# Kernel optimization log

Measured on AMD Instinct MI355X. Metric: run time of the kernel, lower is better.

## Reference

```python
import jax, jax.numpy as jnp
import numpy as np

B, N, P, K, D = 8, 2048, 64, 32, 384
DEPTH, DI, DS, DCONV, DTR, NC = 12, 768, 16, 4, 24, 40
BN_EPS = 1e-5


def _spread_bits(v):
    v = v & 1023
    v = (v | (v << 16)) & 50331903
    v = (v | (v << 8)) & 50393103
    v = (v | (v << 4)) & 51130563
    v = (v | (v << 2)) & 153391689
    return v


def _zkey(x, y, z):
    return _spread_bits(x) | (_spread_bits(y) << 1) | (_spread_bits(z) << 2)


def _sfc_order(xyz, trans):
    lo = xyz.min(0, keepdims=True)
    hi = xyz.max(0, keepdims=True)
    q = jnp.clip(((xyz - lo) / (hi - lo + 1e-6) * 1023.0).astype(jnp.int32), 0, 1023)
    if trans:
        keys = _zkey(q[:, 2], q[:, 1], q[:, 0])
    else:
        keys = _zkey(q[:, 0], q[:, 1], q[:, 2])
    return jnp.argsort(keys)


def _ln(x, g, b):
    m = x.mean(-1, keepdims=True)
    v = jnp.var(x, axis=-1, keepdims=True)
    return (x - m) / jnp.sqrt(v + 1e-5) * g + b


def _bn_eval(x, g, b):
    # BatchNorm in eval mode, running_mean=0 / running_var=1
    return x * (g / np.float32(np.sqrt(1.0 + BN_EPS))) + b


def _patch_embed_one(xyz, w1, b1, g1, be1, w2, b2, g2, be2, w3, b3, g3, be3):
    # xyz: (N,3)
    cidx = (jnp.arange(P) * (N / P)).astype(jnp.int32)
    centers = xyz[cidx]                                      # (P,3)
    d2 = ((centers[:, None, :] - xyz[None, :, :]) ** 2).sum(-1)  # (P,N)
    _, knn = jax.lax.top_k(-d2, K)                           # (P,K) smallest dists
    nx = xyz[knn] - centers[:, None, :]                      # (P,K,3)
    h = jax.nn.gelu(_bn_eval(nx @ w1.T + b1, g1, be1), approximate=False)   # (P,K,64)
    h = jax.nn.gelu(_bn_eval(h @ w2.T + b2, g2, be2), approximate=False)    # (P,K,128)
    h = _bn_eval(h @ w3.T + b3, g3, be3)                     # (P,K,384)
    return h.max(1), centers


def _mamba(x, in_w, conv_w, conv_b, xp_w, dt_w, dt_b, Alog, Dp, out_w):
    # x: (B,L,D)
    Bsz, L, _ = x.shape
    xz = x @ in_w.T                                          # (B,L,2*DI)
    xc, z = xz[..., :DI], xz[..., DI:]
    xpad = jnp.pad(xc, ((0, 0), (DCONV - 1, 0), (0, 0)))
    xc = sum(xpad[:, j:j + L, :] * conv_w[:, j] for j in range(DCONV)) + conv_b
    xc = jax.nn.silu(xc)
    x_dbl = xc @ xp_w.T                                      # (B,L,DTR+2*DS)
    dt = x_dbl[..., :DTR]
    Bm = x_dbl[..., DTR:DTR + DS]
    Cm = x_dbl[..., DTR + DS:]
    delta = jax.nn.softplus(dt @ dt_w.T + dt_b)              # (B,L,DI)
    A = -jnp.exp(Alog)                                       # (DI,DS)

    def step(h, inp):
        d_t, B_t, C_t, u_t = inp                             # (B,DI),(B,DS),(B,DS),(B,DI)
        h = h * jnp.exp(d_t[..., None] * A) + (d_t * u_t)[..., None] * B_t[:, None, :]
        return h, jnp.einsum('bds,bs->bd', h, C_t)

    h0 = jnp.zeros((Bsz, DI, DS), x.dtype)
    inps = (delta.transpose(1, 0, 2), Bm.transpose(1, 0, 2),
            Cm.transpose(1, 0, 2), xc.transpose(1, 0, 2))
    _, ys = jax.lax.scan(step, h0, inps)                     # (L,B,DI)
    y = ys.transpose(1, 0, 2) + Dp * xc
    y = y * jax.nn.silu(z)
    return y @ out_w.T


def setup_inputs() -> dict:
    key = jax.random.key(0)
    ks = iter(jax.random.split(key, 64))
    nrm = lambda *s: jax.random.normal(next(ks), s, jnp.float32) * 0.02
    inp = {
        'data': jax.random.normal(next(ks), (B, N, 3), jnp.float32),
        'pe_w1': nrm(64, 3), 'pe_b1': jnp.zeros(64), 'pe_g1': jnp.ones(64), 'pe_be1': jnp.zeros(64),
        'pe_w2': nrm(128, 64), 'pe_b2': jnp.zeros(128), 'pe_g2': jnp.ones(128), 'pe_be2': jnp.zeros(128),
        'pe_w3': nrm(D, 128), 'pe_b3': jnp.zeros(D), 'pe_g3': jnp.ones(D), 'pe_be3': jnp.zeros(D),
        'oi_h_scale': jnp.ones(D), 'oi_h_shift': jnp.zeros(D),
        'oi_th_scale': jnp.ones(D), 'oi_th_shift': jnp.zeros(D),
        'pos_embed': nrm(1, P, D),
        'blk_ln_g': jnp.ones((DEPTH, D)), 'blk_ln_b': jnp.zeros((DEPTH, D)),
        'blk_in_w': nrm(DEPTH, 2 * DI, D),
        'blk_conv_w': nrm(DEPTH, DI, DCONV), 'blk_conv_b': jnp.zeros((DEPTH, DI)),
        'blk_xp_w': nrm(DEPTH, DTR + 2 * DS, DI),
        'blk_dt_w': nrm(DEPTH, DI, DTR), 'blk_dt_b': jnp.full((DEPTH, DI), -4.0),
        'blk_Alog': jnp.tile(jnp.log(jnp.arange(1, DS + 1, dtype=jnp.float32)), (DEPTH, DI, 1)),
        'blk_D': jnp.ones((DEPTH, DI)),
        'blk_out_w': nrm(DEPTH, D, DI),
        'norm_g': jnp.ones(D), 'norm_b': jnp.zeros(D),
        'mlp_w1': nrm(256, D), 'mlp_b1': jnp.zeros(256),
        'mlp_w2': nrm(64, 256), 'mlp_b2': jnp.zeros(64),
        'mlp_w3': nrm(NC, 64), 'mlp_b3': jnp.zeros(NC),
    }
    return inp


def reference(data, pe_w1, pe_b1, pe_g1, pe_be1, pe_w2, pe_b2, pe_g2, pe_be2,
              pe_w3, pe_b3, pe_g3, pe_be3, oi_h_scale, oi_h_shift, oi_th_scale,
              oi_th_shift, pos_embed, blk_ln_g, blk_ln_b, blk_in_w, blk_conv_w,
              blk_conv_b, blk_xp_w, blk_dt_w, blk_dt_b, blk_Alog, blk_D,
              blk_out_w, norm_g, norm_b, mlp_w1, mlp_b1, mlp_w2, mlp_b2,
              mlp_w3, mlp_b3):
    xyz = data[:, :, :3]
    tokens, centers = jax.vmap(
        _patch_embed_one, in_axes=(0,) + (None,) * 12)(
        xyz, pe_w1, pe_b1, pe_g1, pe_be1, pe_w2, pe_b2, pe_g2, pe_be2,
        pe_w3, pe_b3, pe_g3, pe_be3)                         # (B,P,D),(B,P,3)
    order_h = jax.vmap(lambda c: _sfc_order(c, False))(centers)
    order_th = jax.vmap(lambda c: _sfc_order(c, True))(centers)
    th = jnp.take_along_axis(tokens, order_h[:, :, None], axis=1) * oi_h_scale + oi_h_shift
    tth = jnp.take_along_axis(tokens, order_th[:, :, None], axis=1) * oi_th_scale + oi_th_shift
    t = jnp.concatenate([th + pos_embed, tth + pos_embed], axis=1)  # (B,2P,D)
    for i in range(DEPTH):
        t = t + _mamba(_ln(t, blk_ln_g[i], blk_ln_b[i]),
                       blk_in_w[i], blk_conv_w[i], blk_conv_b[i], blk_xp_w[i],
                       blk_dt_w[i], blk_dt_b[i], blk_Alog[i], blk_D[i], blk_out_w[i])
    t = _ln(t, norm_g, norm_b)
    x = t.mean(1)
    x = jax.nn.relu(x @ mlp_w1.T + mlp_b1)
    x = jax.nn.relu(x @ mlp_w2.T + mlp_b2)
    return x @ mlp_w3.T + mlp_b3
```

## Files before the change

kernel.cpp:

```cpp
#include <hip/hip_runtime.h>
#include <math.h>

#define BB 8
#define NN 2048
#define PP 64
#define KK 32
#define DD 384
#define DEPTH 12
#define DI 768
#define DS 16
#define DCONV 4
#define DTR 24
#define NC 40
#define LL 128
#define XROW (DTR + 2 * DS)
#define NR (BB * LL)
#define XPARTS 12

using bf16x8 = __attribute__((ext_vector_type(8))) short;
using floatx4 = __attribute__((ext_vector_type(4))) float;

__device__ __forceinline__ float gelu_exact(float x) {
    return 0.5f * x * (1.0f + erff(x * 0.70710678118654752440f));
}
__device__ __forceinline__ float siluf(float x) {
    return x / (1.0f + expf(-x));
}
__device__ __forceinline__ unsigned short f2bf(float f) {
    unsigned u = __float_as_uint(f);
    u += 0x7fffu + ((u >> 16) & 1u);
    return (unsigned short)(u >> 16);
}
__device__ __forceinline__ float bf2f(short s) {
    return __uint_as_float(((unsigned)(unsigned short)s) << 16);
}
__device__ __forceinline__ unsigned spread_bits(unsigned v) {
    v &= 1023u;
    v = (v | (v << 16)) & 50331903u;
    v = (v | (v << 8)) & 50393103u;
    v = (v | (v << 4)) & 51130563u;
    v = (v | (v << 2)) & 153391689u;
    return v;
}

__global__ void k_cvt(const float* __restrict__ in_w, const float* __restrict__ out_w,
                      const float* __restrict__ pe_w3, const float* __restrict__ xp,
                      unsigned short* __restrict__ inwbf, unsigned short* __restrict__ owbf,
                      unsigned short* __restrict__ w3bf, unsigned short* __restrict__ xpbf)
{
    int idx = blockIdx.x * 256 + threadIdx.x;
    const int n1 = DEPTH * 2 * DI * DD;
    const int n2 = DEPTH * DD * DI;
    const int n3 = DD * 128;
    const int n4 = DEPTH * 64 * DI;
    if (idx < n1) { inwbf[idx] = f2bf(in_w[idx]); return; }
    idx -= n1;
    if (idx < n2) { owbf[idx] = f2bf(out_w[idx]); return; }
    idx -= n2;
    if (idx < n3) { w3bf[idx] = f2bf(pe_w3[idx]); return; }
    idx -= n3;
    if (idx < n4) {
        int i = idx / (64 * DI);
        int rem = idx - i * 64 * DI;
        int n = rem / DI, k = rem % DI;
        float v = (n < XROW) ? xp[(size_t)i * XROW * DI + (size_t)n * DI + k] : 0.f;
        xpbf[idx] = f2bf(v);
    }
}

__global__ __launch_bounds__(256) void k_knn(const float* __restrict__ data,
                                             int* __restrict__ knn_out,
                                             float* __restrict__ centers)
{
    const int bp = blockIdx.x;
    const int b = bp >> 6, p = bp & 63;
    const int tid = threadIdx.x;
    const int lane = tid & 63, wid = tid >> 6;
    const float* X = data + (size_t)b * NN * 3;

    const float cx = X[p * 32 * 3 + 0];
    const float cy = X[p * 32 * 3 + 1];
    const float cz = X[p * 32 * 3 + 2];
    if (tid == 0) {
        centers[(b * PP + p) * 3 + 0] = cx;
        centers[(b * PP + p) * 3 + 1] = cy;
        centers[(b * PP + p) * 3 + 2] = cz;
    }

    unsigned long long pk[8];
#pragma unroll
    for (int q = 0; q < 8; q++) {
        int i = tid + 256 * q;
        float dx = cx - X[i * 3 + 0];
        float dy = cy - X[i * 3 + 1];
        float dz = cz - X[i * 3 + 2];
        float d2 = dx * dx + dy * dy + dz * dz;
        pk[q] = ((unsigned long long)__float_as_uint(d2) << 32) | (unsigned)i;
    }

    __shared__ unsigned long long wred[4];
    __shared__ int klist[KK];
    for (int k = 0; k < KK; k++) {
        unsigned long long m = pk[0];
#pragma unroll
        for (int q = 1; q < 8; q++) m = pk[q] < m ? pk[q] : m;
#pragma unroll
        for (int off = 32; off; off >>= 1) {
            unsigned long long o = __shfl_xor(m, off);
            m = o < m ? o : m;
        }
        if (lane == 0) wred[wid] = m;
        __syncthreads();
        unsigned long long g = wred[0];
#pragma unroll
        for (int w = 1; w < 4; w++) g = wred[w] < g ? wred[w] : g;
#pragma unroll
        for (int q = 0; q < 8; q++)
            if (pk[q] == g) pk[q] = ~0ull;
        if (tid == 0) klist[k] = (int)(g & 0xffffffffu);
        __syncthreads();
    }
    if (tid < KK) knn_out[bp * KK + tid] = klist[tid];
}

__global__ __launch_bounds__(256) void k_pe_mlp(
    const float* __restrict__ data, const int* __restrict__ knn_in,
    const float* __restrict__ w1, const float* __restrict__ b1,
    const float* __restrict__ g1, const float* __restrict__ be1,
    const float* __restrict__ w2, const float* __restrict__ b2,
    const float* __restrict__ g2, const float* __restrict__ be2,
    const unsigned short* __restrict__ w3bf, const float* __restrict__ b3,
    const float* __restrict__ g3, const float* __restrict__ be3,
    float* __restrict__ tokens)
{
    const int bp = blockIdx.x;
    const int b = bp >> 6, p = bp & 63;
    const int tid = threadIdx.x;
    const float* X = data + (size_t)b * NN * 3;
    const float inv_den = 0.99999500003749968752f;

    __shared__ float nxs[KK * 3];
    __shared__ float h1s[KK * 64];
    __shared__ short h2b[KK * 136];

    const float cx = X[p * 32 * 3 + 0];
    const float cy = X[p * 32 * 3 + 1];
    const float cz = X[p * 32 * 3 + 2];
    if (tid < KK) {
        int q = knn_in[bp * KK + tid];
        nxs[tid * 3 + 0] = X[q * 3 + 0] - cx;
        nxs[tid * 3 + 1] = X[q * 3 + 1] - cy;
        nxs[tid * 3 + 2] = X[q * 3 + 2] - cz;
    }
    __syncthreads();

    for (int e = tid; e < KK * 64; e += 256) {
        int j = e >> 6, c = e & 63;
        float v = nxs[j * 3 + 0] * w1[c * 3 + 0] + nxs[j * 3 + 1] * w1[c * 3 + 1] +
                  nxs[j * 3 + 2] * w1[c * 3 + 2] + b1[c];
        v = v * (g1[c] * inv_den) + be1[c];
        h1s[j * 64 + c] = gelu_exact(v);
    }
    __syncthreads();

    for (int e = tid; e < KK * 128; e += 256) {
        int j = e >> 7, c = e & 127;
        const float4* wr = (const float4*)(w2 + (size_t)c * 64);
        const float4* hr = (const float4*)(h1s + j * 64);
        float acc = 0.f;
#pragma unroll
        for (int q = 0; q < 16; q++) {
            float4 wv = wr[q], hv = hr[q];
            acc += hv.x * wv.x + hv.y * wv.y + hv.z * wv.z + hv.w * wv.w;
        }
        float v = (acc + b2[c]) * (g2[c] * inv_den) + be2[c];
        h2b[j * 136 + c] = (short)f2bf(gelu_exact(v));
    }
    __syncthreads();

    const int wave = tid >> 6, lane = tid & 63;
    const int quad = lane >> 4, r = lane & 15;
    floatx4 acc3[2][6] = {};
#pragma unroll
    for (int ks = 0; ks < 4; ks++) {
        const int k0 = ks * 32;
        bf16x8 af[2];
        af[0] = *(const bf16x8*)(h2b + (size_t)r * 136 + quad * 8 + k0);
        af[1] = *(const bf16x8*)(h2b + (size_t)(16 + r) * 136 + quad * 8 + k0);
        bf16x8 bfv[6];
#pragma unroll
        for (int nj = 0; nj < 6; nj++) {
            int n = wave * 96 + nj * 16 + r;
            bfv[nj] = *(const bf16x8*)(w3bf + (size_t)n * 128 + quad * 8 + k0);
        }
#pragma unroll
        for (int mi = 0; mi < 2; mi++)
#pragma unroll
            for (int nj = 0; nj < 6; nj++)
                acc3[mi][nj] = __builtin_amdgcn_mfma_f32_16x16x32_bf16(af[mi], bfv[nj], acc3[mi][nj], 0, 0, 0);
    }
#pragma unroll
    for (int nj = 0; nj < 6; nj++) {
        int col = wave * 96 + nj * 16 + r;
        float sc = g3[col] * inv_den;
        float offc = b3[col] * sc + be3[col];
        float m = -3.4e38f;
#pragma unroll
        for (int mi = 0; mi < 2; mi++)
#pragma unroll
            for (int r2 = 0; r2 < 4; r2++)
                m = fmaxf(m, acc3[mi][nj][r2] * sc + offc);
        m = fmaxf(m, __shfl_xor(m, 16));
        m = fmaxf(m, __shfl_xor(m, 32));
        if (quad == 0) tokens[(size_t)bp * DD + col] = m;
    }
}

__global__ __launch_bounds__(64) void k_sfc(const float* __restrict__ centers,
                                            int* __restrict__ order_h,
                                            int* __restrict__ order_th)
{
    const int b = blockIdx.x;
    const int tid = threadIdx.x;
    float cc[3];
    cc[0] = centers[(b * PP + tid) * 3 + 0];
    cc[1] = centers[(b * PP + tid) * 3 + 1];
    cc[2] = centers[(b * PP + tid) * 3 + 2];

    __shared__ float csh[PP][3];
    __shared__ float slo[3], shi[3];
    csh[tid][0] = cc[0]; csh[tid][1] = cc[1]; csh[tid][2] = cc[2];
    __syncthreads();
    if (tid == 0) {
        for (int k = 0; k < 3; k++) {
            float lo = csh[0][k], hi = csh[0][k];
            for (int j = 1; j < PP; j++) { lo = fminf(lo, csh[j][k]); hi = fmaxf(hi, csh[j][k]); }
            slo[k] = lo; shi[k] = hi;
        }
    }
    __syncthreads();

    int q[3];
    for (int k = 0; k < 3; k++) {
        float t = (cc[k] - slo[k]) / (shi[k] - slo[k] + 1e-6f) * 1023.0f;
        int qi = (int)t;
        qi = qi < 0 ? 0 : (qi > 1023 ? 1023 : qi);
        q[k] = qi;
    }
    unsigned kh = spread_bits((unsigned)q[0]) | (spread_bits((unsigned)q[1]) << 1) |
                  (spread_bits((unsigned)q[2]) << 2);
    unsigned kt = spread_bits((unsigned)q[2]) | (spread_bits((unsigned)q[1]) << 1) |
                  (spread_bits((unsigned)q[0]) << 2);

    __shared__ unsigned khs[PP], kts[PP];
    khs[tid] = kh; kts[tid] = kt;
    __syncthreads();
    int rh = 0, rt = 0;
    for (int j = 0; j < PP; j++) {
        unsigned a = khs[j];
        rh += (a < kh) || (a == kh && j < tid);
        unsigned c = kts[j];
        rt += (c < kt) || (c == kt && j < tid);
    }
    order_h[b * PP + rh] = tid;
    order_th[b * PP + rt] = tid;
}

__global__ void k_build_t(const float* __restrict__ tokens,
                          const int* __restrict__ order_h, const int* __restrict__ order_th,
                          const float* __restrict__ hs, const float* __restrict__ hb,
                          const float* __restrict__ ts, const float* __restrict__ tb,
                          const float* __restrict__ pos, float* __restrict__ t)
{
    int idx = blockIdx.x * blockDim.x + threadIdx.x;
    if (idx >= BB * LL * DD) return;
    int d = idx % DD;
    int l = (idx / DD) % LL;
    int b = idx / (DD * LL);
    float v;
    if (l < PP) {
        int src = order_h[b * PP + l];
        v = tokens[((size_t)b * PP + src) * DD + d] * hs[d] + hb[d] + pos[l * DD + d];
    } else {
        int ll2 = l - PP;
        int src = order_th[b * PP + ll2];
        v = tokens[((size_t)b * PP + src) * DD + d] * ts[d] + tb[d] + pos[ll2 * DD + d];
    }
    t[idx] = v;
}

__global__ __launch_bounds__(256) void k_stats(const float* __restrict__ t,
                                               const float* __restrict__ g,
                                               const float* __restrict__ gb,
                                               unsigned short* __restrict__ tbf)
{
    const int tid = threadIdx.x;
    const int wid = tid >> 6, lane = tid & 63;
    const int row = blockIdx.x * 4 + wid;
    const size_t base = (size_t)row * DD;
    float v[6];
    float s = 0.f, q = 0.f;
#pragma unroll
    for (int j = 0; j < 6; j++) {
        v[j] = t[base + lane + 64 * j];
        s += v[j]; q += v[j] * v[j];
    }
#pragma unroll
    for (int off = 32; off; off >>= 1) { s += __shfl_xor(s, off); q += __shfl_xor(q, off); }
    float mean = s * (1.0f / DD);
    float var = q * (1.0f / DD) - mean * mean;
    float inv = 1.0f / sqrtf(var + 1e-5f);
#pragma unroll
    for (int j = 0; j < 6; j++) {
        int i = lane + 64 * j;
        tbf[base + i] = f2bf((v[j] - mean) * inv * g[i] + gb[i]);
    }
}

__global__ __launch_bounds__(256) void k_mfma_xz(
    const unsigned short* __restrict__ tbf,
    const unsigned short* __restrict__ inwbf,
    const float* __restrict__ cw, const float* __restrict__ cb,
    const unsigned short* __restrict__ xpbf,
    unsigned short* __restrict__ xcbf, unsigned short* __restrict__ zsbf,
    float* __restrict__ parts_x)
{
    __shared__ short ct[128][72];
    const int tid = threadIdx.x;
    const int wave = tid >> 6, lane = tid & 63;
    const int quad = lane >> 4, r = lane & 15;
    const int wm = wave >> 1, wn = wave & 1;
    const int b = blockIdx.y;
    const int n0 = blockIdx.x * 64;
    const int m0 = b * 128 + wm * 64;

    floatx4 acc[4][2] = {};
    const unsigned short* Ab = tbf + (size_t)(m0 + r) * DD + quad * 8;
    const unsigned short* Bb = inwbf + (size_t)(n0 + wn * 32 + r) * DD + quad * 8;
    for (int k0 = 0; k0 < DD; k0 += 32) {
        bf16x8 af[4], bfv[2];
#pragma unroll
        for (int i = 0; i < 4; i++)
            af[i] = *(const bf16x8*)(Ab + (size_t)(i * 16) * DD + k0);
#pragma unroll
        for (int j = 0; j < 2; j++)
            bfv[j] = *(const bf16x8*)(Bb + (size_t)(j * 16) * DD + k0);
#pragma unroll
        for (int i = 0; i < 4; i++)
#pragma unroll
            for (int j = 0; j < 2; j++)
                acc[i][j] = __builtin_amdgcn_mfma_f32_16x16x32_bf16(af[i], bfv[j], acc[i][j], 0, 0, 0);
    }

#pragma unroll
    for (int i = 0; i < 4; i++)
#pragma unroll
        for (int r2 = 0; r2 < 4; r2++) {
            short* cp = &ct[wm * 64 + i * 16 + quad * 4 + r2][wn * 32 + r];
#pragma unroll
            for (int j = 0; j < 2; j++)
                cp[j * 16] = (short)f2bf(acc[i][j][r2]);
        }
    __syncthreads();

    const int l0 = (tid >> 3) * 4;
    const int c0 = (tid & 7) * 8;
    if (n0 < DI) {
        float cwv[8][4], cbv[8];
#pragma unroll
        for (int q = 0; q < 8; q++) {
            *(float4*)cwv[q] = *(const float4*)(cw + (size_t)(n0 + c0 + q) * 4);
            cbv[q] = cb[n0 + c0 + q];
        }
        unsigned short ov[4][8];
#pragma unroll
        for (int dl = 0; dl < 4; dl++) {
            const int l = l0 + dl;
            float u[8];
#pragma unroll
            for (int q = 0; q < 8; q++) u[q] = cbv[q];
#pragma unroll
            for (int j = 0; j < DCONV; j++) {
                int lt = l - (DCONV - 1) + j;
                if (lt >= 0) {
                    bf16x8 x = *(const bf16x8*)&ct[lt][c0];
#pragma unroll
                    for (int q = 0; q < 8; q++) u[q] += bf2f(x[q]) * cwv[q][j];
                }
            }
#pragma unroll
            for (int q = 0; q < 8; q++) ov[dl][q] = f2bf(siluf(u[q]));
        }
        __syncthreads();
#pragma unroll
        for (int dl = 0; dl < 4; dl++) {
            const int l = l0 + dl;
            *(bf16x8*)&ct[l][c0] = *(bf16x8*)ov[dl];
            *(bf16x8*)(xcbf + (size_t)(b * LL + l) * DI + n0 + c0) = *(bf16x8*)ov[dl];
        }
        __syncthreads();

        const int zi = blockIdx.x;
        floatx4 acc2[2][4] = {};
#pragma unroll
        for (int k0 = 0; k0 < 64; k0 += 32) {
            bf16x8 af2[2], bfv2[4];
#pragma unroll
            for (int i = 0; i < 2; i++)
                af2[i] = *(const bf16x8*)&ct[wave * 32 + i * 16 + r][k0 + quad * 8];
#pragma unroll
            for (int nj = 0; nj < 4; nj++)
                bfv2[nj] = *(const bf16x8*)(xpbf + (size_t)(nj * 16 + r) * DI + n0 + k0 + quad * 8);
#pragma unroll
            for (int i = 0; i < 2; i++)
#pragma unroll
                for (int nj = 0; nj < 4; nj++)
                    acc2[i][nj] = __builtin_amdgcn_mfma_f32_16x16x32_bf16(af2[i], bfv2[nj], acc2[i][nj], 0, 0, 0);
        }
        float* out = parts_x + (size_t)zi * NR * XROW;
#pragma unroll
        for (int i = 0; i < 2; i++)
#pragma unroll
            for (int nj = 0; nj < 4; nj++) {
                int col = nj * 16 + r;
                if (col < XROW) {
#pragma unroll
                    for (int r2 = 0; r2 < 4; r2++) {
                        int row = b * LL + wave * 32 + i * 16 + quad * 4 + r2;
                        out[(size_t)row * XROW + col] = acc2[i][nj][r2];
                    }
                }
            }
    } else {
        const int nz = n0 - DI;
#pragma unroll
        for (int dl = 0; dl < 4; dl++) {
            const int l = l0 + dl;
            bf16x8 x = *(const bf16x8*)&ct[l][c0];
            unsigned short o[8];
#pragma unroll
            for (int q = 0; q < 8; q++) o[q] = f2bf(siluf(bf2f(x[q])));
            *(bf16x8*)(zsbf + (size_t)(b * LL + l) * DI + nz + c0) = *(bf16x8*)o;
        }
    }
}

__global__ void k_xred(const float* __restrict__ parts, float* __restrict__ xdbl)
{
    int i = blockIdx.x * 256 + threadIdx.x;
    if (i >= NR * XROW) return;
    float s = 0.f;
#pragma unroll
    for (int z = 0; z < XPARTS; z++) s += parts[(size_t)z * NR * XROW + i];
    xdbl[i] = s;
}

__global__ __launch_bounds__(128) void k_scan(
    const float* __restrict__ xdbl,
    const unsigned short* __restrict__ xcbf, const unsigned short* __restrict__ zsbf,
    const float* __restrict__ dtw, const float* __restrict__ dtb,
    const float* __restrict__ Alog, const float* __restrict__ Dp,
    unsigned short* __restrict__ ybf)
{
    const int tid = threadIdx.x;
    const int b = blockIdx.x / DI;
    const int d = blockIdx.x % DI;

    __shared__ float da[LL][17];
    __shared__ float Bsh[LL][17];
    __shared__ float Csh[LL][17];
    __shared__ float dus[LL];
    __shared__ float us[LL];
    __shared__ float zs[LL];
    __shared__ float ApL[DS][9];
    __shared__ float HlL[DS][9];
    __shared__ float hst[DS][9];

    {
        const int t = tid;
        const size_t row = (size_t)b * LL + t;
        const float* xd = xdbl + row * XROW;
        const float* w = dtw + d * DTR;
        float acc = dtb[d];
#pragma unroll
        for (int k = 0; k < DTR; k++) acc += xd[k] * w[k];
        float delta = fmaxf(acc, 0.f) + log1pf(__expf(-fabsf(acc)));
        float u = bf2f((short)xcbf[row * DI + d]);
        dus[t] = delta * u;
        us[t] = u;
        zs[t] = bf2f((short)zsbf[row * DI + d]);
#pragma unroll
        for (int s = 0; s < DS; s++) {
            da[t][s] = __expf(delta * (-__expf(Alog[d * DS + s])));
            Bsh[t][s] = xd[DTR + s];
            Csh[t][s] = xd[DTR + DS + s];
        }
    }
    __syncthreads();

    const int s = tid & 15;
    const int c = tid >> 4;

    {
        float h = 0.f, Ap = 1.f;
#pragma unroll
        for (int q = 0; q < 16; q++) {
            int t = c * 16 + q;
            float a = da[t][s];
            h = h * a + dus[t] * Bsh[t][s];
            Ap *= a;
        }
        ApL[s][c] = Ap;
        HlL[s][c] = h;
    }
    __syncthreads();
    if (tid < DS) {
        float hs = 0.f;
#pragma unroll
        for (int cc = 0; cc < 8; cc++) {
            hst[tid][cc] = hs;
            hs = ApL[tid][cc] * hs + HlL[tid][cc];
        }
    }
    __syncthreads();

    {
        const float Dd = Dp[d];
        float h = hst[s][c];
        unsigned short* yc = ybf + ((size_t)b * LL + c * 16) * DI + d;
#pragma unroll
        for (int q = 0; q < 16; q++) {
            int t = c * 16 + q;
            float a = da[t][s];
            h = h * a + dus[t] * Bsh[t][s];
            float p = h * Csh[t][s];
            p += __shfl_xor(p, 1, 16);
            p += __shfl_xor(p, 2, 16);
            p += __shfl_xor(p, 4, 16);
            p += __shfl_xor(p, 8, 16);
            if (s == 0) yc[(size_t)q * DI] = f2bf((p + Dd * us[t]) * zs[t]);
        }
    }
}

__global__ __launch_bounds__(256) void k_mfma_op(
    const unsigned short* __restrict__ ybf,
    const unsigned short* __restrict__ owbf,
    float* __restrict__ t)
{
    const int tid = threadIdx.x;
    const int wave = tid >> 6, lane = tid & 63;
    const int quad = lane >> 4, r = lane & 15;
    const int wr2 = wave >> 1, wc = wave & 1;
    const int n0 = blockIdx.x * 64 + wc * 32;
    const int m0 = blockIdx.y * 32 + wr2 * 16;

    floatx4 acc[2] = {};
    const unsigned short* Ab = ybf + (size_t)(m0 + r) * DI + quad * 8;
    const unsigned short* Bb = owbf + (size_t)(n0 + r) * DI + quad * 8;
    for (int k0 = 0; k0 < DI; k0 += 32) {
        bf16x8 af = *(const bf16x8*)(Ab + k0);
        bf16x8 b0 = *(const bf16x8*)(Bb + k0);
        bf16x8 b1 = *(const bf16x8*)(Bb + (size_t)16 * DI + k0);
        acc[0] = __builtin_amdgcn_mfma_f32_16x16x32_bf16(af, b0, acc[0], 0, 0, 0);
        acc[1] = __builtin_amdgcn_mfma_f32_16x16x32_bf16(af, b1, acc[1], 0, 0, 0);
    }

#pragma unroll
    for (int j = 0; j < 2; j++) {
        int col = n0 + j * 16 + r;
#pragma unroll
        for (int r2 = 0; r2 < 4; r2++) {
            int row = m0 + quad * 4 + r2;
            float* tp = t + (size_t)row * DD + col;
            *tp += acc[j][r2];
        }
    }
}

__global__ __launch_bounds__(256) void k_lnpool(const float* __restrict__ t,
                                                const float* __restrict__ ng,
                                                const float* __restrict__ nb,
                                                float* __restrict__ pparts)
{
    const int b = blockIdx.y, chunk = blockIdx.x;
    const int tid = threadIdx.x;
    const int wave = tid >> 6, lane = tid & 63;
    __shared__ float pw[4][DD];

    for (int c = lane; c < DD; c += 64) pw[wave][c] = 0.f;
    __syncthreads();

    for (int rr = 0; rr < 4; rr++) {
        const int row = b * LL + chunk * 16 + wave * 4 + rr;
        const float* xr = t + (size_t)row * DD;
        float v[6];
        float s = 0.f, q = 0.f;
#pragma unroll
        for (int j = 0; j < 6; j++) { v[j] = xr[lane + 64 * j]; s += v[j]; q += v[j] * v[j]; }
#pragma unroll
        for (int off = 32; off; off >>= 1) { s += __shfl_xor(s, off); q += __shfl_xor(q, off); }
        float mean = s * (1.0f / DD);
        float var = q * (1.0f / DD) - mean * mean;
        float inv = 1.0f / sqrtf(var + 1e-5f);
#pragma unroll
        for (int j = 0; j < 6; j++) {
            int c = lane + 64 * j;
            pw[wave][c] += (v[j] - mean) * inv * ng[c] + nb[c];
        }
    }
    __syncthreads();
    float* out = pparts + ((size_t)b * 8 + chunk) * DD;
    for (int c = tid; c < DD; c += 256)
        out[c] = pw[0][c] + pw[1][c] + pw[2][c] + pw[3][c];
}

__global__ __launch_bounds__(256) void k_mlp(const float* __restrict__ pparts,
    const float* __restrict__ w1, const float* __restrict__ b1,
    const float* __restrict__ w2, const float* __restrict__ b2,
    const float* __restrict__ w3, const float* __restrict__ b3,
    float* __restrict__ out)
{
    const int b = blockIdx.x, tid = threadIdx.x;
    __shared__ float pl[DD];
    __shared__ float h1[256];
    __shared__ float h2[64];
    for (int c = tid; c < DD; c += 256) {
        const float* pp = pparts + (size_t)b * 8 * DD + c;
        float s = 0.f;
#pragma unroll
        for (int z = 0; z < 8; z++) s += pp[z * DD];
        pl[c] = s * (1.0f / LL);
    }
    __syncthreads();

    {
        float acc = b1[tid];
        const float* wr = w1 + (size_t)tid * DD;
        for (int k = 0; k < DD; k++) acc += pl[k] * wr[k];
        h1[tid] = fmaxf(acc, 0.f);
    }
    __syncthreads();
    if (tid < 64) {
        float acc = b2[tid];
        const float* wr = w2 + (size_t)tid * 256;
        for (int k = 0; k < 256; k++) acc += h1[k] * wr[k];
        h2[tid] = fmaxf(acc, 0.f);
    }
    __syncthreads();
    if (tid < NC) {
        float acc = b3[tid];
        const float* wr = w3 + (size_t)tid * 64;
        for (int k = 0; k < 64; k++) acc += h2[k] * wr[k];
        out[b * NC + tid] = acc;
    }
}

extern "C" void kernel_launch(void* const* d_in, const int* in_sizes, int n_in,
                              void* d_out, int out_size, void* d_ws, size_t ws_size,
                              hipStream_t stream)
{
    const float* data      = (const float*)d_in[0];
    const float* pe_w1     = (const float*)d_in[1];
    const float* pe_b1     = (const float*)d_in[2];
    const float* pe_g1     = (const float*)d_in[3];
    const float* pe_be1    = (const float*)d_in[4];
    const float* pe_w2     = (const float*)d_in[5];
    const float* pe_b2     = (const float*)d_in[6];
    const float* pe_g2     = (const float*)d_in[7];
    const float* pe_be2    = (const float*)d_in[8];
    const float* pe_w3     = (const float*)d_in[9];
    const float* pe_b3     = (const float*)d_in[10];
    const float* pe_g3     = (const float*)d_in[11];
    const float* pe_be3    = (const float*)d_in[12];
    const float* oi_h_scale  = (const float*)d_in[13];
    const float* oi_h_shift  = (const float*)d_in[14];
    const float* oi_th_scale = (const float*)d_in[15];
    const float* oi_th_shift = (const float*)d_in[16];
    const float* pos_embed = (const float*)d_in[17];
    const float* blk_ln_g  = (const float*)d_in[18];
    const float* blk_ln_b  = (const float*)d_in[19];
    const float* blk_in_w  = (const float*)d_in[20];
    const float* blk_conv_w = (const float*)d_in[21];
    const float* blk_conv_b = (const float*)d_in[22];
    const float* blk_xp_w  = (const float*)d_in[23];
    const float* blk_dt_w  = (const float*)d_in[24];
    const float* blk_dt_b  = (const float*)d_in[25];
    const float* blk_Alog  = (const float*)d_in[26];
    const float* blk_D     = (const float*)d_in[27];
    const float* blk_out_w = (const float*)d_in[28];
    const float* norm_g    = (const float*)d_in[29];
    const float* norm_b    = (const float*)d_in[30];
    const float* mlp_w1    = (const float*)d_in[31];
    const float* mlp_b1    = (const float*)d_in[32];
    const float* mlp_w2    = (const float*)d_in[33];
    const float* mlp_b2    = (const float*)d_in[34];
    const float* mlp_w3    = (const float*)d_in[35];
    const float* mlp_b3    = (const float*)d_in[36];

    float* ws = (float*)d_ws;
    size_t off = 0;
    auto alloc = [&](size_t n) { float* p = ws + off; off += (n + 63) & ~(size_t)63; return p; };
    float* tokens  = alloc((size_t)BB * PP * DD);
    float* centers = alloc((size_t)BB * PP * 3);
    int*   order_h = (int*)alloc((size_t)BB * PP);
    int*   order_th= (int*)alloc((size_t)BB * PP);
    int*   knn_idx = (int*)alloc((size_t)BB * PP * KK);
    float* t    = alloc((size_t)NR * DD);
    float* xdbl = alloc((size_t)NR * XROW);
    float* parts_x = alloc((size_t)XPARTS * NR * XROW);
    float* pparts  = alloc((size_t)BB * 8 * DD);
    unsigned short* tbf   = (unsigned short*)alloc((size_t)NR * DD / 2);
    unsigned short* xcbf  = (unsigned short*)alloc((size_t)NR * DI / 2);
    unsigned short* zsbf  = (unsigned short*)alloc((size_t)NR * DI / 2);
    unsigned short* ybf   = (unsigned short*)alloc((size_t)NR * DI / 2);
    unsigned short* inwbf = (unsigned short*)alloc((size_t)DEPTH * 2 * DI * DD / 2);
    unsigned short* owbf  = (unsigned short*)alloc((size_t)DEPTH * DD * DI / 2);
    unsigned short* xpbf  = (unsigned short*)alloc((size_t)DEPTH * 64 * DI / 2);
    unsigned short* w3bf  = (unsigned short*)alloc((size_t)DD * 128 / 2);

    {
        const int total = DEPTH * 2 * DI * DD + DEPTH * DD * DI + DD * 128 + DEPTH * 64 * DI;
        k_cvt<<<(total + 255) / 256, 256, 0, stream>>>(
            blk_in_w, blk_out_w, pe_w3, blk_xp_w, inwbf, owbf, w3bf, xpbf);
    }

    k_knn<<<BB * PP, 256, 0, stream>>>(data, knn_idx, centers);
    k_pe_mlp<<<BB * PP, 256, 0, stream>>>(data, knn_idx,
        pe_w1, pe_b1, pe_g1, pe_be1, pe_w2, pe_b2, pe_g2, pe_be2,
        w3bf, pe_b3, pe_g3, pe_be3, tokens);
    k_sfc<<<BB, 64, 0, stream>>>(centers, order_h, order_th);
    {
        int nt = BB * LL * DD;
        k_build_t<<<(nt + 255) / 256, 256, 0, stream>>>(tokens, order_h, order_th,
            oi_h_scale, oi_h_shift, oi_th_scale, oi_th_shift, pos_embed, t);
    }

    for (int i = 0; i < DEPTH; i++) {
        const float* ln_g = blk_ln_g + i * DD;
        const float* ln_b = blk_ln_b + i * DD;
        const float* cw   = blk_conv_w + (size_t)i * DI * DCONV;
        const float* cb   = blk_conv_b + (size_t)i * DI;
        const float* dtw  = blk_dt_w + (size_t)i * DI * DTR;
        const float* dtb  = blk_dt_b + (size_t)i * DI;
        const float* Al   = blk_Alog + (size_t)i * DI * DS;
        const float* Dpp  = blk_D + (size_t)i * DI;
        const unsigned short* inw = inwbf + (size_t)i * 2 * DI * DD;
        const unsigned short* ow  = owbf + (size_t)i * DD * DI;
        const unsigned short* xpb = xpbf + (size_t)i * 64 * DI;

        k_stats<<<NR / 4, 256, 0, stream>>>(t, ln_g, ln_b, tbf);
        k_mfma_xz<<<dim3(24, BB), 256, 0, stream>>>(
            tbf, inw, cw, cb, xpb, xcbf, zsbf, parts_x);
        k_xred<<<(NR * XROW + 255) / 256, 256, 0, stream>>>(parts_x, xdbl);
        k_scan<<<BB * DI, 128, 0, stream>>>(xdbl, xcbf, zsbf, dtw, dtb, Al, Dpp, ybf);
        k_mfma_op<<<dim3(DD / 64, NR / 32), 256, 0, stream>>>(ybf, ow, t);
    }

    k_lnpool<<<dim3(8, BB), 256, 0, stream>>>(t, norm_g, norm_b, pparts);
    k_mlp<<<BB, 256, 0, stream>>>(pparts, mlp_w1, mlp_b1, mlp_w2, mlp_b2, mlp_w3, mlp_b3,
                                  (float*)d_out);
}
```

Baseline: 1.043 ms.

## Replace partial-sum reduction kernel with atomics and fuse SFC ordering into token build

The x-projection partials are now accumulated directly into xdbl with atomicAdd, and the LayerNorm stats kernel zeroes the buffer first. This removes the per-layer reduction kernel and the partials buffer. The SFC ordering kernel is merged into the token build kernel, which recomputes the ordering per block. This saves launches and memory traffic, but adds atomic contention and makes the float summation order nondeterministic.

```diff
diff --git a/kernel.cpp b/kernel.cpp
--- a/kernel.cpp
+++ b/kernel.cpp
@@ -15,7 +15,6 @@
 #define LL 128
 #define XROW (DTR + 2 * DS)
 #define NR (BB * LL)
-#define XPARTS 12
 
 using bf16x8 = __attribute__((ext_vector_type(8))) short;
 using floatx4 = __attribute__((ext_vector_type(4))) float;
@@ -216,20 +215,25 @@
     }
 }
 
-__global__ __launch_bounds__(64) void k_sfc(const float* __restrict__ centers,
-                                            int* __restrict__ order_h,
-                                            int* __restrict__ order_th)
-{
-    const int b = blockIdx.x;
+__global__ __launch_bounds__(256) void k_build_t(
+    const float* __restrict__ tokens, const float* __restrict__ centers,
+    const float* __restrict__ hs, const float* __restrict__ hb,
+    const float* __restrict__ ts, const float* __restrict__ tb,
+    const float* __restrict__ pos, float* __restrict__ t)
+{
+    const int b = blockIdx.y, chunk = blockIdx.x;
     const int tid = threadIdx.x;
-    float cc[3];
-    cc[0] = centers[(b * PP + tid) * 3 + 0];
-    cc[1] = centers[(b * PP + tid) * 3 + 1];
-    cc[2] = centers[(b * PP + tid) * 3 + 2];
 
     __shared__ float csh[PP][3];
     __shared__ float slo[3], shi[3];
-    csh[tid][0] = cc[0]; csh[tid][1] = cc[1]; csh[tid][2] = cc[2];
+    __shared__ unsigned khs[PP], kts[PP];
+    __shared__ int ordh[PP], ordth[PP];
+
+    if (tid < PP) {
+        csh[tid][0] = centers[(b * PP + tid) * 3 + 0];
+        csh[tid][1] = centers[(b * PP + tid) * 3 + 1];
+        csh[tid][2] = centers[(b * PP + tid) * 3 + 2];
+    }
     __syncthreads();
     if (tid == 0) {
         for (int k = 0; k < 3; k++) {
@@ -239,62 +243,61 @@
         }
     }
     __syncthreads();
-
-    int q[3];
-    for (int k = 0; k < 3; k++) {
-        float t = (cc[k] - slo[k]) / (shi[k] - slo[k] + 1e-6f) * 1023.0f;
-        int qi = (int)t;
-        qi = qi < 0 ? 0 : (qi > 1023 ? 1023 : qi);
-        q[k] = qi;
-    }
-    unsigned kh = spread_bits((unsigned)q[0]) | (spread_bits((unsigned)q[1]) << 1) |
-                  (spread_bits((unsigned)q[2]) << 2);
-    unsigned kt = spread_bits((unsigned)q[2]) | (spread_bits((unsigned)q[1]) << 1) |
-                  (spread_bits((unsigned)q[0]) << 2);
-
-    __shared__ unsigned khs[PP], kts[PP];
-    khs[tid] = kh; kts[tid] = kt;
-    __syncthreads();
-    int rh = 0, rt = 0;
-    for (int j = 0; j < PP; j++) {
-        unsigned a = khs[j];
-        rh += (a < kh) || (a == kh && j < tid);
-        unsigned c = kts[j];
-        rt += (c < kt) || (c == kt && j < tid);
-    }
-    order_h[b * PP + rh] = tid;
-    order_th[b * PP + rt] = tid;
-}
-
-__global__ void k_build_t(const float* __restrict__ tokens,
-                          const int* __restrict__ order_h, const int* __restrict__ order_th,
-                          const float* __restrict__ hs, const float* __restrict__ hb,
-                          const float* __restrict__ ts, const float* __restrict__ tb,
-                          const float* __restrict__ pos, float* __restrict__ t)
-{
-    int idx = blockIdx.x * blockDim.x + threadIdx.x;
-    if (idx >= BB * LL * DD) return;
-    int d = idx % DD;
-    int l = (idx / DD) % LL;
-    int b = idx / (DD * LL);
-    float v;
-    if (l < PP) {
-        int src = order_h[b * PP + l];
-        v = tokens[((size_t)b * PP + src) * DD + d] * hs[d] + hb[d] + pos[l * DD + d];
-    } else {
-        int ll2 = l - PP;
-        int src = order_th[b * PP + ll2];
-        v = tokens[((size_t)b * PP + src) * DD + d] * ts[d] + tb[d] + pos[ll2 * DD + d];
-    }
-    t[idx] = v;
+    if (tid < PP) {
+        int q[3];
+        for (int k = 0; k < 3; k++) {
+            float v = (csh[tid][k] - slo[k]) / (shi[k] - slo[k] + 1e-6f) * 1023.0f;
+            int qi = (int)v;
+            qi = qi < 0 ? 0 : (qi > 1023 ? 1023 : qi);
+            q[k] = qi;
+        }
+        khs[tid] = spread_bits((unsigned)q[0]) | (spread_bits((unsigned)q[1]) << 1) |
+                   (spread_bits((unsigned)q[2]) << 2);
+        kts[tid] = spread_bits((unsigned)q[2]) | (spread_bits((unsigned)q[1]) << 1) |
+                   (spread_bits((unsigned)q[0]) << 2);
+    }
+    __syncthreads();
+    if (tid < PP) {
+        unsigned kh = khs[tid], kt = kts[tid];
+        int rh = 0, rt = 0;
+        for (int j = 0; j < PP; j++) {
+            unsigned a = khs[j];
+            rh += (a < kh) || (a == kh && j < tid);
+            unsigned c = kts[j];
+            rt += (c < kt) || (c == kt && j < tid);
+        }
+        ordh[rh] = tid;
+        ordth[rt] = tid;
+    }
+    __syncthreads();
+
+    for (int e = tid; e < 8 * DD; e += 256) {
+        const int l = chunk * 8 + (e / DD);
+        const int d = e % DD;
+        float v;
+        if (l < PP) {
+            int src = ordh[l];
+            v = tokens[((size_t)b * PP + src) * DD + d] * hs[d] + hb[d] + pos[l * DD + d];
+        } else {
+            int l2 = l - PP;
+            int src = ordth[l2];
+            v = tokens[((size_t)b * PP + src) * DD + d] * ts[d] + tb[d] + pos[l2 * DD + d];
+        }
+        t[((size_t)b * LL + l) * DD + d] = v;
+    }
 }
 
 __global__ __launch_bounds__(256) void k_stats(const float* __restrict__ t,
                                                const float* __restrict__ g,
                                                const float* __restrict__ gb,
-                                               unsigned short* __restrict__ tbf)
+                                               unsigned short* __restrict__ tbf,
+                                               float* __restrict__ xdbl)
 {
     const int tid = threadIdx.x;
+    {
+        int zi = blockIdx.x * 224 + tid;
+        if (tid < 224) xdbl[zi] = 0.f;
+    }
     const int wid = tid >> 6, lane = tid & 63;
     const int row = blockIdx.x * 4 + wid;
     const size_t base = (size_t)row * DD;
@@ -323,7 +326,7 @@
     const float* __restrict__ cw, const float* __restrict__ cb,
     const unsigned short* __restrict__ xpbf,
     unsigned short* __restrict__ xcbf, unsigned short* __restrict__ zsbf,
-    float* __restrict__ parts_x)
+    float* __restrict__ xdbl)
 {
     __shared__ short ct[128][72];
     const int tid = threadIdx.x;
@@ -400,7 +403,6 @@
         }
         __syncthreads();
 
-        const int zi = blockIdx.x;
         floatx4 acc2[2][4] = {};
 #pragma unroll
         for (int k0 = 0; k0 < 64; k0 += 32) {
@@ -417,7 +419,6 @@
                 for (int nj = 0; nj < 4; nj++)
                     acc2[i][nj] = __builtin_amdgcn_mfma_f32_16x16x32_bf16(af2[i], bfv2[nj], acc2[i][nj], 0, 0, 0);
         }
-        float* out = parts_x + (size_t)zi * NR * XROW;
 #pragma unroll
         for (int i = 0; i < 2; i++)
 #pragma unroll
@@ -427,7 +428,7 @@
 #pragma unroll
                     for (int r2 = 0; r2 < 4; r2++) {
                         int row = b * LL + wave * 32 + i * 16 + quad * 4 + r2;
-                        out[(size_t)row * XROW + col] = acc2[i][nj][r2];
+                        atomicAdd(&xdbl[(size_t)row * XROW + col], acc2[i][nj][r2]);
                     }
                 }
             }
@@ -443,16 +444,6 @@
             *(bf16x8*)(zsbf + (size_t)(b * LL + l) * DI + nz + c0) = *(bf16x8*)o;
         }
     }
-}
-
-__global__ void k_xred(const float* __restrict__ parts, float* __restrict__ xdbl)
-{
-    int i = blockIdx.x * 256 + threadIdx.x;
-    if (i >= NR * XROW) return;
-    float s = 0.f;
-#pragma unroll
-    for (int z = 0; z < XPARTS; z++) s += parts[(size_t)z * NR * XROW + i];
-    xdbl[i] = s;
 }
 
 __global__ __launch_bounds__(128) void k_scan(
@@ -703,12 +694,9 @@
     auto alloc = [&](size_t n) { float* p = ws + off; off += (n + 63) & ~(size_t)63; return p; };
     float* tokens  = alloc((size_t)BB * PP * DD);
     float* centers = alloc((size_t)BB * PP * 3);
-    int*   order_h = (int*)alloc((size_t)BB * PP);
-    int*   order_th= (int*)alloc((size_t)BB * PP);
     int*   knn_idx = (int*)alloc((size_t)BB * PP * KK);
     float* t    = alloc((size_t)NR * DD);
     float* xdbl = alloc((size_t)NR * XROW);
-    float* parts_x = alloc((size_t)XPARTS * NR * XROW);
     float* pparts  = alloc((size_t)BB * 8 * DD);
     unsigned short* tbf   = (unsigned short*)alloc((size_t)NR * DD / 2);
     unsigned short* xcbf  = (unsigned short*)alloc((size_t)NR * DI / 2);
@@ -729,12 +717,8 @@
     k_pe_mlp<<<BB * PP, 256, 0, stream>>>(data, knn_idx,
         pe_w1, pe_b1, pe_g1, pe_be1, pe_w2, pe_b2, pe_g2, pe_be2,
         w3bf, pe_b3, pe_g3, pe_be3, tokens);
-    k_sfc<<<BB, 64, 0, stream>>>(centers, order_h, order_th);
-    {
-        int nt = BB * LL * DD;
-        k_build_t<<<(nt + 255) / 256, 256, 0, stream>>>(tokens, order_h, order_th,
-            oi_h_scale, oi_h_shift, oi_th_scale, oi_th_shift, pos_embed, t);
-    }
+    k_build_t<<<dim3(16, BB), 256, 0, stream>>>(tokens, centers,
+        oi_h_scale, oi_h_shift, oi_th_scale, oi_th_shift, pos_embed, t);
 
     for (int i = 0; i < DEPTH; i++) {
         const float* ln_g = blk_ln_g + i * DD;
@@ -749,10 +733,9 @@
         const unsigned short* ow  = owbf + (size_t)i * DD * DI;
         const unsigned short* xpb = xpbf + (size_t)i * 64 * DI;
 
-        k_stats<<<NR / 4, 256, 0, stream>>>(t, ln_g, ln_b, tbf);
+        k_stats<<<NR / 4, 256, 0, stream>>>(t, ln_g, ln_b, tbf, xdbl);
         k_mfma_xz<<<dim3(24, BB), 256, 0, stream>>>(
-            tbf, inw, cw, cb, xpb, xcbf, zsbf, parts_x);
-        k_xred<<<(NR * XROW + 255) / 256, 256, 0, stream>>>(parts_x, xdbl);
+            tbf, inw, cw, cb, xpb, xcbf, zsbf, xdbl);
         k_scan<<<BB * DI, 128, 0, stream>>>(xdbl, xcbf, zsbf, dtw, dtb, Al, Dpp, ybf);
         k_mfma_op<<<dim3(DD / 64, NR / 32), 256, 0, stream>>>(ybf, ow, t);
     }
```

After: 1.058 ms. No clear change (+1.4%).
